# Optimization experiments

Hardware: AMD Instinct MI355X
Metric: run time of the kernel (lower is better)

## Reference

```python
import jax, jax.numpy as jnp
import numpy as np

RADIUS = 1.3
N_SAMPLES = 256
STEP = 0.0176


def trilinear(grid, pts):
    """grid: [C, D, H, W]; pts: [M, 3] in [-1, 1] ordered (x, y, z) like torch grid_sample
    (x indexes W, y indexes H, z indexes D), align_corners=True, border padding.
    Returns [M, C]."""
    C, D, H, W = grid.shape
    sizes = jnp.asarray([W, H, D], dtype=pts.dtype)
    co = jnp.clip((pts + 1.0) * 0.5 * (sizes - 1.0), 0.0, sizes - 1.0)
    c0 = jnp.floor(co)
    f = co - c0                                   # [M,3] trilinear weights
    i0 = c0.astype(jnp.int32)
    i1 = jnp.minimum(i0 + 1, jnp.asarray([W - 1, H - 1, D - 1], jnp.int32))
    gf = grid.reshape(C, -1)

    def gat(ix, iy, iz):                          # -> [M, C]
        return gf[:, (iz * H + iy) * W + ix].T

    x0, y0, z0 = i0[:, 0], i0[:, 1], i0[:, 2]
    x1, y1, z1 = i1[:, 0], i1[:, 1], i1[:, 2]
    wx, wy, wz = f[:, 0:1], f[:, 1:2], f[:, 2:3]
    out = (gat(x0, y0, z0) * (1 - wx) * (1 - wy) * (1 - wz)
         + gat(x1, y0, z0) * wx       * (1 - wy) * (1 - wz)
         + gat(x0, y1, z0) * (1 - wx) * wy       * (1 - wz)
         + gat(x1, y1, z0) * wx       * wy       * (1 - wz)
         + gat(x0, y0, z1) * (1 - wx) * (1 - wy) * wz
         + gat(x1, y0, z1) * wx       * (1 - wy) * wz
         + gat(x0, y1, z1) * (1 - wx) * wy       * wz
         + gat(x1, y1, z1) * wx       * wy       * wz)
    return out


def get_intersections(rays_o, dirn):
    """Ray / cube[-R,R]^3 intersection; N_SAMPLES uniform steps from entry point.
    Returns pts [B,N,3], t-values [B,N], validity mask [B,N]."""
    eps = 1e-9
    safe_d = jnp.where(jnp.abs(dirn) < eps, eps, dirn)
    inv = 1.0 / safe_d
    t1 = (-RADIUS - rays_o) * inv
    t2 = (RADIUS - rays_o) * inv
    tmin = jnp.max(jnp.minimum(t1, t2), axis=-1)
    tmax = jnp.min(jnp.maximum(t1, t2), axis=-1)
    tnear = jnp.maximum(tmin, 0.0)
    hit = tmax > tnear                                          # [B]
    t = tnear[:, None] + STEP * jnp.arange(N_SAMPLES, dtype=rays_o.dtype)[None, :]
    pts = rays_o[:, None, :] + t[..., None] * dirn[:, None, :]  # [B,N,3]
    mask = (t < tmax[:, None]) & hit[:, None]
    return pts, t, mask


def setup_inputs() -> dict:
    key = jax.random.key(0)
    ks = jax.random.split(key, 12)
    B, R, GD, FD, NF, HW = 2048, 128, 3, 32, 32, 64
    o = jax.random.normal(ks[0], (B, 3), dtype=jnp.float32)
    rays_o = o / jnp.linalg.norm(o, axis=-1, keepdims=True) * (2.0 * RADIUS)
    rays_d = -rays_o + 0.3 * jax.random.normal(ks[1], (B, 3), dtype=jnp.float32)
    G1 = 0.01 * jax.random.normal(ks[2], (GD, R, R, R), dtype=jnp.float32)
    F = 0.05 * jax.random.normal(ks[3], (FD, NF, NF, NF), dtype=jnp.float32)
    s = 0.1
    return {
        'rays_o': rays_o, 'rays_d': rays_d, 'G1': G1, 'F': F,
        'Wd1': s * jax.random.normal(ks[4], (FD, HW), dtype=jnp.float32),
        'bd1': jnp.zeros((HW,), jnp.float32),
        'Wd2': s * jax.random.normal(ks[5], (HW, 1), dtype=jnp.float32),
        'bd2': jnp.zeros((1,), jnp.float32),
        'Wc1': s * jax.random.normal(ks[6], (FD + 3, HW), dtype=jnp.float32),
        'bc1': jnp.zeros((HW,), jnp.float32),
        'Wc2': s * jax.random.normal(ks[7], (HW, 3), dtype=jnp.float32),
        'bc2': jnp.zeros((3,), jnp.float32),
    }


def reference(rays_o, rays_d, G1, F, Wd1, bd1, Wd2, bd2, Wc1, bc1, Wc2, bc2):
    B = rays_o.shape[0]
    dirn = rays_d / jnp.linalg.norm(rays_d, axis=-1, keepdims=True)
    pts, t, mask = get_intersections(rays_o, dirn)           # [B,N,3],[B,N],[B,N]
    pts_n = (pts / RADIUS).reshape(-1, 3)                     # [M,3] in ~[-1,1]

    # nested multi-grid trilinear lookups: coords -> G1 -> F
    g1v = trilinear(G1, pts_n)                                # [M,3]
    feats = trilinear(F, g1v)                                 # [M,feature_dim]

    # density MLP (1 hidden layer, width 64)
    h = jax.nn.relu(feats @ Wd1 + bd1)
    sigma = (h @ Wd2 + bd2)[:, 0].reshape(B, N_SAMPLES)
    sigma = jnp.where(mask, sigma, 0.0)

    # sigma -> alpha -> compositing weights (abs_light)
    dists = jnp.concatenate([t[:, 1:] - t[:, :-1],
                             jnp.full((B, 1), STEP, t.dtype)], axis=1)
    alpha = 1.0 - jnp.exp(-jax.nn.relu(sigma) * dists)
    T = jnp.cumprod(1.0 - alpha + 1e-10, axis=1)
    T_excl = jnp.concatenate([jnp.ones((B, 1), alpha.dtype), T[:, :-1]], axis=1)
    weights = alpha * T_excl                                  # [B,N]

    # color MLP conditioned on view direction
    dflat = jnp.broadcast_to(dirn[:, None, :], (B, N_SAMPLES, 3)).reshape(-1, 3)
    hc = jax.nn.relu(jnp.concatenate([feats, dflat], axis=-1) @ Wc1 + bc1)
    rgb = jax.nn.sigmoid((hc @ Wc2 + bc2).reshape(B, N_SAMPLES, 3))
    rgb = jnp.where(mask[..., None], rgb, 0.0)

    out = jnp.sum(weights[..., None] * rgb, axis=1)           # [B,3]
    acc = jnp.sum(weights, axis=1)
    return out + (1.0 - acc)[:, None]                         # white background
```

## Files before the change

### kernel.cpp

```cpp
#include <hip/hip_runtime.h>
#include <hip/hip_fp16.h>
#include <math.h>

#define NSAMP 256

typedef _Float16 f16;
typedef _Float16 f16x4 __attribute__((ext_vector_type(4)));
typedef _Float16 f16x8 __attribute__((ext_vector_type(8)));
typedef float    f32x4 __attribute__((ext_vector_type(4)));

__global__ __launch_bounds__(256) void transpose_F16(
    const float* __restrict__ Fg, f16* __restrict__ Ft)
{
    const int j = blockIdx.x * 256 + threadIdx.x;
    f16x8 o[4];
    #pragma unroll
    for (int q = 0; q < 4; ++q)
        #pragma unroll
        for (int i = 0; i < 8; ++i)
            o[q][i] = (f16)Fg[(size_t)(8*q+i)*32768 + j];
    f16* dst = Ft + (size_t)j * 32;
    #pragma unroll
    for (int q = 0; q < 4; ++q) *(f16x8*)(dst + q*8) = o[q];
    if (j == 32767) {
        f16x8 z = {};
        f16* pd = Ft + (size_t)32768 * 32;
        #pragma unroll
        for (int q = 0; q < 4; ++q) *(f16x8*)(pd + q*8) = z;
    }
}

__global__ __launch_bounds__(256) void transpose_G1p(
    const float* __restrict__ G1, f16x8* __restrict__ G1p)
{
    const int v  = blockIdx.x * 256 + threadIdx.x;
    const int vn = min(v + 1, 2097151);
    f16x8 o;
    o[0] = (f16)G1[v];
    o[1] = (f16)G1[2097152 + v];
    o[2] = (f16)G1[2*2097152 + v];
    o[3] = (f16)0.0f;
    o[4] = (f16)G1[vn];
    o[5] = (f16)G1[2097152 + vn];
    o[6] = (f16)G1[2*2097152 + vn];
    o[7] = (f16)0.0f;
    G1p[v] = o;
}

__global__ __launch_bounds__(256) void pack_bfrags(
    const float* __restrict__ Wd1, const float* __restrict__ Wc1,
    f16* __restrict__ Bd, f16* __restrict__ Bc)
{
    const int idx  = threadIdx.x;
    const int nt   = idx >> 6;
    const int lane = idx & 63;
    const int j    = nt*16 + (lane & 15);
    const int k0   = (lane >> 4) * 8;
    f16x8 vd, vc;
    #pragma unroll
    for (int i = 0; i < 8; ++i) {
        vd[i] = (f16)Wd1[(k0+i)*64 + j];
        vc[i] = (f16)Wc1[(k0+i)*64 + j];
    }
    *(f16x8*)(Bd + ((size_t)(nt*64+lane))*8) = vd;
    *(f16x8*)(Bc + ((size_t)(nt*64+lane))*8) = vc;
}

__global__ __launch_bounds__(256) __attribute__((amdgpu_waves_per_eu(2, 6)))
void nerf_fused_opt(
    const float* __restrict__ rays_o, const float* __restrict__ rays_d,
    const f16x8* __restrict__ G1p, const f16* __restrict__ Ft16,
    const float* __restrict__ bd1, const float* __restrict__ Wd2,
    const float* __restrict__ bd2,
    const float* __restrict__ Wc1, const float* __restrict__ bc1,
    const float* __restrict__ Wc2, const float* __restrict__ bc2,
    const f16* __restrict__ Bd, const f16* __restrict__ Bc,
    float* __restrict__ out)
{
    const float RADIUS = 1.3f;
    const float STEP = 0.0176f;

    const int b    = blockIdx.x;
    const int tid  = threadIdx.x;
    const int lane = tid & 63;
    const int wv   = tid >> 6;

    __shared__ __align__(16) f16 feats_lds[256][40];
    __shared__ float sig_lds[256];
    __shared__ f16   rgb_lds[256][4];
    __shared__ float s_wtot[4];
    __shared__ float s_red[4][4];

    const float ox = rays_o[b*3+0], oy = rays_o[b*3+1], oz = rays_o[b*3+2];
    const float rdx = rays_d[b*3+0], rdy = rays_d[b*3+1], rdz = rays_d[b*3+2];
    const float rn  = sqrtf(rdx*rdx + rdy*rdy + rdz*rdz);
    const float dxn = rdx/rn, dyn = rdy/rn, dzn = rdz/rn;

    float sd, inv, t1, t2, tmin, tmax;
    sd = (fabsf(dxn) < 1e-9f) ? 1e-9f : dxn; inv = 1.0f/sd;
    t1 = (-RADIUS - ox)*inv; t2 = (RADIUS - ox)*inv;
    tmin = fminf(t1,t2); tmax = fmaxf(t1,t2);
    sd = (fabsf(dyn) < 1e-9f) ? 1e-9f : dyn; inv = 1.0f/sd;
    t1 = (-RADIUS - oy)*inv; t2 = (RADIUS - oy)*inv;
    tmin = fmaxf(tmin, fminf(t1,t2)); tmax = fminf(tmax, fmaxf(t1,t2));
    sd = (fabsf(dzn) < 1e-9f) ? 1e-9f : dzn; inv = 1.0f/sd;
    t1 = (-RADIUS - oz)*inv; t2 = (RADIUS - oz)*inv;
    tmin = fmaxf(tmin, fminf(t1,t2)); tmax = fminf(tmax, fmaxf(t1,t2));

    const float tnear = fmaxf(tmin, 0.0f);
    const bool  hit   = tmax > tnear;
    const float t     = tnear + STEP * (float)tid;
    const bool  mask  = (t < tmax) && hit;

    const bool wave_active = __any(mask);

    float sigma = 0.0f, rr = 0.0f, rg = 0.0f, rb = 0.0f;

    float feats[32];
    if (wave_active) {
        const float invR = 1.0f / RADIUS;
        const float px = (ox + t*dxn) * invR;
        const float py = (oy + t*dyn) * invR;
        const float pz = (oz + t*dzn) * invR;

        float cox = fminf(fmaxf((px+1.0f)*0.5f*127.0f, 0.0f), 127.0f);
        float coy = fminf(fmaxf((py+1.0f)*0.5f*127.0f, 0.0f), 127.0f);
        float coz = fminf(fmaxf((pz+1.0f)*0.5f*127.0f, 0.0f), 127.0f);
        int x0 = (int)floorf(cox); float fx = cox - (float)x0;
        int y0 = (int)floorf(coy); float fy = coy - (float)y0; int y1 = min(y0+1, 127);
        int z0 = (int)floorf(coz); float fz = coz - (float)z0; int z1 = min(z0+1, 127);

        {
            const float wx0 = 1.0f-fx, wx1 = fx;
            const float wy0 = 1.0f-fy, wy1 = fy;
            const float wz0 = 1.0f-fz, wz1 = fz;
            const int i000 = (z0*128 + y0)*128 + x0;
            const int dyo = (y1 - y0)*128;
            const int dzo = (z1 - z0)*16384;

            const f16x8 p00 = G1p[i000];
            const f16x8 p10 = G1p[i000 + dyo];
            const f16x8 p01 = G1p[i000 + dzo];
            const f16x8 p11 = G1p[i000 + dyo + dzo];

            const float a00 = wy0*wz0, a10 = wy1*wz0, a01 = wy0*wz1, a11 = wy1*wz1;

            float g[3];
            #pragma unroll
            for (int c = 0; c < 3; ++c) {
                g[c] = a00*(wx0*(float)p00[c] + wx1*(float)p00[4+c])
                     + a10*(wx0*(float)p10[c] + wx1*(float)p10[4+c])
                     + a01*(wx0*(float)p01[c] + wx1*(float)p01[4+c])
                     + a11*(wx0*(float)p11[c] + wx1*(float)p11[4+c]);
            }

            cox = fminf(fmaxf((g[0]+1.0f)*0.5f*31.0f, 0.0f), 31.0f);
            coy = fminf(fmaxf((g[1]+1.0f)*0.5f*31.0f, 0.0f), 31.0f);
            coz = fminf(fmaxf((g[2]+1.0f)*0.5f*31.0f, 0.0f), 31.0f);
            x0 = (int)floorf(cox); fx = cox - (float)x0;
            y0 = (int)floorf(coy); fy = coy - (float)y0; y1 = min(y0+1, 31);
            z0 = (int)floorf(coz); fz = coz - (float)z0; z1 = min(z0+1, 31);
        }

        #pragma unroll
        for (int c = 0; c < 32; ++c) feats[c] = 0.0f;
        {
            const float wx0 = 1.0f-fx, wx1 = fx;
            const float wy0 = 1.0f-fy, wy1 = fy;
            const float wz0 = 1.0f-fz, wz1 = fz;
            const int j000 = (z0*32 + y0)*32 + x0;
            const int dyo = (y1 - y0)*32;
            const int dzo = (z1 - z0)*1024;

            const int   jp[4] = { j000, j000+dyo, j000+dzo, j000+dyo+dzo };
            const float ap[4] = { wy0*wz0, wy1*wz0, wy0*wz1, wy1*wz1 };

            #pragma unroll
            for (int p = 0; p < 4; ++p) {
                const f16* base = Ft16 + (size_t)jp[p] * 32;
                const float aw = ap[p]*wx0, bw = ap[p]*wx1;
                f16x8 lo[4], hi[4];
                #pragma unroll
                for (int q = 0; q < 4; ++q) lo[q] = *(const f16x8*)(base + q*8);
                #pragma unroll
                for (int q = 0; q < 4; ++q) hi[q] = *(const f16x8*)(base + 32 + q*8);
                #pragma unroll
                for (int q = 0; q < 4; ++q)
                    #pragma unroll
                    for (int i = 0; i < 8; ++i)
                        feats[8*q+i] += aw*(float)lo[q][i] + bw*(float)hi[q][i];
            }
        }
    }

    if (wave_active) {
        #pragma unroll
        for (int gq = 0; gq < 4; ++gq) {
            f16x8 h;
            #pragma unroll
            for (int i = 0; i < 8; ++i) h[i] = (f16)feats[gq*8+i];
            *(f16x8*)&feats_lds[tid][gq*8] = h;
        }
    }
    __syncthreads();

    if (wave_active) {
        const int lane15 = lane & 15;
        const int laneg  = lane >> 4;

        float bias_d[4], bias_c[4], wd2v[4];
        float wc2r[4], wc2g[4], wc2b[4];
        #pragma unroll
        for (int nt = 0; nt < 4; ++nt) {
            const int j = nt*16 + lane15;
            bias_d[nt] = bd1[j];
            bias_c[nt] = bc1[j] + dxn*Wc1[32*64+j] + dyn*Wc1[33*64+j] + dzn*Wc1[34*64+j];
            wd2v[nt]   = Wd2[j];
            wc2r[nt]   = Wc2[j*3+0];
            wc2g[nt]   = Wc2[j*3+1];
            wc2b[nt]   = Wc2[j*3+2];
        }
        f16x8 bdf[4], bcf[4];
        #pragma unroll
        for (int nt = 0; nt < 4; ++nt) {
            bdf[nt] = *(const f16x8*)(Bd + ((size_t)(nt*64+lane))*8);
            bcf[nt] = *(const f16x8*)(Bc + ((size_t)(nt*64+lane))*8);
        }

        #pragma unroll
        for (int mt = 0; mt < 4; ++mt) {
            const int arow = wv*64 + mt*16 + lane15;
            const f16x8 af = *(const f16x8*)&feats_lds[arow][laneg*8];

            f32x4 accd[4], accc[4];
            #pragma unroll
            for (int nt = 0; nt < 4; ++nt) {
                const float bdv = bias_d[nt], bcv = bias_c[nt];
                accd[nt] = (f32x4){bdv, bdv, bdv, bdv};
                accc[nt] = (f32x4){bcv, bcv, bcv, bcv};
            }
            #pragma unroll
            for (int nt = 0; nt < 4; ++nt) {
                accd[nt] = __builtin_amdgcn_mfma_f32_16x16x32_f16(af, bdf[nt], accd[nt], 0, 0, 0);
                accc[nt] = __builtin_amdgcn_mfma_f32_16x16x32_f16(af, bcf[nt], accc[nt], 0, 0, 0);
            }

            float ss[4] = {0.f,0.f,0.f,0.f};
            float sr[4] = {0.f,0.f,0.f,0.f};
            float sg[4] = {0.f,0.f,0.f,0.f};
            float sb[4] = {0.f,0.f,0.f,0.f};
            #pragma unroll
            for (int nt = 0; nt < 4; ++nt) {
                #pragma unroll
                for (int reg = 0; reg < 4; ++reg) {
                    const float hd = fmaxf(accd[nt][reg], 0.0f);
                    ss[reg] += hd * wd2v[nt];
                    const float hc = fmaxf(accc[nt][reg], 0.0f);
                    sr[reg] += hc * wc2r[nt];
                    sg[reg] += hc * wc2g[nt];
                    sb[reg] += hc * wc2b[nt];
                }
            }
            #pragma unroll
            for (int st = 1; st < 16; st <<= 1) {
                #pragma unroll
                for (int reg = 0; reg < 4; ++reg) {
                    ss[reg] += __shfl_xor(ss[reg], st, 64);
                    sr[reg] += __shfl_xor(sr[reg], st, 64);
                    sg[reg] += __shfl_xor(sg[reg], st, 64);
                    sb[reg] += __shfl_xor(sb[reg], st, 64);
                }
            }
            if (lane15 == 0) {
                const int base = wv*64 + mt*16 + laneg*4;
                #pragma unroll
                for (int reg = 0; reg < 4; ++reg) {
                    sig_lds[base+reg]    = ss[reg];
                    rgb_lds[base+reg][0] = (f16)sr[reg];
                    rgb_lds[base+reg][1] = (f16)sg[reg];
                    rgb_lds[base+reg][2] = (f16)sb[reg];
                }
            }
        }
    }
    __syncthreads();

    {
        const float sv  = sig_lds[tid];
        const float crv = (float)rgb_lds[tid][0] + bc2[0];
        const float cgv = (float)rgb_lds[tid][1] + bc2[1];
        const float cbv = (float)rgb_lds[tid][2] + bc2[2];
        sigma = mask ? (sv + bd2[0]) : 0.0f;
        rr = mask ? 1.0f/(1.0f + expf(-crv)) : 0.0f;
        rg = mask ? 1.0f/(1.0f + expf(-cgv)) : 0.0f;
        rb = mask ? 1.0f/(1.0f + expf(-cbv)) : 0.0f;
    }

    const float alpha = 1.0f - expf(-fmaxf(sigma, 0.0f) * STEP);
    float p = 1.0f - alpha + 1e-10f;

    float scan = p;
    #pragma unroll
    for (int off = 1; off < 64; off <<= 1) {
        const float n = __shfl_up(scan, off, 64);
        if (lane >= off) scan *= n;
    }
    if (lane == 63) s_wtot[wv] = scan;
    __syncthreads();

    float pre = 1.0f;
    #pragma unroll
    for (int q = 0; q < 4; ++q) if (q < wv) pre *= s_wtot[q];
    float excl = __shfl_up(scan, 1, 64);
    if (lane == 0) excl = 1.0f;
    const float Texcl = pre * excl;

    const float w = alpha * Texcl;
    float sw  = w;
    float swr = w * rr, swg = w * rg, swb = w * rb;

    #pragma unroll
    for (int off = 32; off > 0; off >>= 1) {
        sw  += __shfl_down(sw,  off, 64);
        swr += __shfl_down(swr, off, 64);
        swg += __shfl_down(swg, off, 64);
        swb += __shfl_down(swb, off, 64);
    }
    if (lane == 0) {
        s_red[wv][0] = sw;  s_red[wv][1] = swr;
        s_red[wv][2] = swg; s_red[wv][3] = swb;
    }
    __syncthreads();
    if (tid == 0) {
        float W = 0.0f, R = 0.0f, Gc = 0.0f, Bc_ = 0.0f;
        #pragma unroll
        for (int q = 0; q < 4; ++q) {
            W  += s_red[q][0]; R  += s_red[q][1];
            Gc += s_red[q][2]; Bc_ += s_red[q][3];
        }
        const float bg = 1.0f - W;
        out[b*3+0] = R   + bg;
        out[b*3+1] = Gc  + bg;
        out[b*3+2] = Bc_ + bg;
    }
}

__global__ __launch_bounds__(256) __attribute__((amdgpu_waves_per_eu(2, 6)))
void nerf_fused_naive(
    const float* __restrict__ rays_o, const float* __restrict__ rays_d,
    const float* __restrict__ G1, const float* __restrict__ Fg,
    const float* __restrict__ Wd1, const float* __restrict__ bd1,
    const float* __restrict__ Wd2, const float* __restrict__ bd2,
    const float* __restrict__ Wc1, const float* __restrict__ bc1,
    const float* __restrict__ Wc2, const float* __restrict__ bc2,
    float* __restrict__ out)
{
    const float RADIUS = 1.3f;
    const float STEP = 0.0176f;

    const int b    = blockIdx.x;
    const int tid  = threadIdx.x;
    const int lane = tid & 63;
    const int wv   = tid >> 6;

    __shared__ float s_wtot[4];
    __shared__ float s_red[4][4];

    const float ox = rays_o[b*3+0], oy = rays_o[b*3+1], oz = rays_o[b*3+2];
    const float rdx = rays_d[b*3+0], rdy = rays_d[b*3+1], rdz = rays_d[b*3+2];
    const float rn  = sqrtf(rdx*rdx + rdy*rdy + rdz*rdz);
    const float dxn = rdx/rn, dyn = rdy/rn, dzn = rdz/rn;

    float sd, inv, t1, t2, tmin, tmax;
    sd = (fabsf(dxn) < 1e-9f) ? 1e-9f : dxn; inv = 1.0f/sd;
    t1 = (-RADIUS - ox)*inv; t2 = (RADIUS - ox)*inv;
    tmin = fminf(t1,t2); tmax = fmaxf(t1,t2);
    sd = (fabsf(dyn) < 1e-9f) ? 1e-9f : dyn; inv = 1.0f/sd;
    t1 = (-RADIUS - oy)*inv; t2 = (RADIUS - oy)*inv;
    tmin = fmaxf(tmin, fminf(t1,t2)); tmax = fminf(tmax, fmaxf(t1,t2));
    sd = (fabsf(dzn) < 1e-9f) ? 1e-9f : dzn; inv = 1.0f/sd;
    t1 = (-RADIUS - oz)*inv; t2 = (RADIUS - oz)*inv;
    tmin = fmaxf(tmin, fminf(t1,t2)); tmax = fminf(tmax, fmaxf(t1,t2));

    const float tnear = fmaxf(tmin, 0.0f);
    const bool  hit   = tmax > tnear;
    const float t     = tnear + STEP * (float)tid;
    const bool  mask  = (t < tmax) && hit;

    float sigma = 0.0f, rr = 0.0f, rg = 0.0f, rb = 0.0f;

    if (__any(mask)) {
        const float invR = 1.0f / RADIUS;
        const float px = (ox + t*dxn) * invR;
        const float py = (oy + t*dyn) * invR;
        const float pz = (oz + t*dzn) * invR;

        float cox = fminf(fmaxf((px+1.0f)*0.5f*127.0f, 0.0f), 127.0f);
        float coy = fminf(fmaxf((py+1.0f)*0.5f*127.0f, 0.0f), 127.0f);
        float coz = fminf(fmaxf((pz+1.0f)*0.5f*127.0f, 0.0f), 127.0f);
        int x0 = (int)floorf(cox); float fx = cox - (float)x0; int x1 = min(x0+1, 127);
        int y0 = (int)floorf(coy); float fy = coy - (float)y0; int y1 = min(y0+1, 127);
        int z0 = (int)floorf(coz); float fz = coz - (float)z0; int z1 = min(z0+1, 127);

        float feats[32];
        {
            const float wx0 = 1.0f-fx, wx1 = fx;
            const float wy0 = 1.0f-fy, wy1 = fy;
            const float wz0 = 1.0f-fz, wz1 = fz;
            const float w000 = wx0*wy0*wz0, w100 = wx1*wy0*wz0;
            const float w010 = wx0*wy1*wz0, w110 = wx1*wy1*wz0;
            const float w001 = wx0*wy0*wz1, w101 = wx1*wy0*wz1;
            const float w011 = wx0*wy1*wz1, w111 = wx1*wy1*wz1;
            const int i000 = (z0*128 + y0)*128 + x0;
            const int dxo = x1 - x0;
            const int dyo = (y1 - y0)*128;
            const int dzo = (z1 - z0)*16384;
            const int i100 = i000 + dxo,       i010 = i000 + dyo;
            const int i110 = i000 + dyo + dxo, i001 = i000 + dzo;
            const int i101 = i000 + dzo + dxo, i011 = i000 + dzo + dyo;
            const int i111 = i000 + dzo + dyo + dxo;

            float g[3];
            #pragma unroll
            for (int c = 0; c < 3; ++c) {
                const float* gp = G1 + (size_t)c * 2097152;
                g[c] = w000*gp[i000] + w100*gp[i100] + w010*gp[i010] + w110*gp[i110]
                     + w001*gp[i001] + w101*gp[i101] + w011*gp[i011] + w111*gp[i111];
            }

            cox = fminf(fmaxf((g[0]+1.0f)*0.5f*31.0f, 0.0f), 31.0f);
            coy = fminf(fmaxf((g[1]+1.0f)*0.5f*31.0f, 0.0f), 31.0f);
            coz = fminf(fmaxf((g[2]+1.0f)*0.5f*31.0f, 0.0f), 31.0f);
            x0 = (int)floorf(cox); fx = cox - (float)x0; x1 = min(x0+1, 31);
            y0 = (int)floorf(coy); fy = coy - (float)y0; y1 = min(y0+1, 31);
            z0 = (int)floorf(coz); fz = coz - (float)z0; z1 = min(z0+1, 31);

            const float vx0 = 1.0f-fx, vx1 = fx;
            const float vy0 = 1.0f-fy, vy1 = fy;
            const float vz0 = 1.0f-fz, vz1 = fz;
            const float u000 = vx0*vy0*vz0, u100 = vx1*vy0*vz0;
            const float u010 = vx0*vy1*vz0, u110 = vx1*vy1*vz0;
            const float u001 = vx0*vy0*vz1, u101 = vx1*vy0*vz1;
            const float u011 = vx0*vy1*vz1, u111 = vx1*vy1*vz1;
            const int j000 = (z0*32 + y0)*32 + x0;
            const int exo = x1 - x0;
            const int eyo = (y1 - y0)*32;
            const int ezo = (z1 - z0)*1024;
            const int j100 = j000 + exo,       j010 = j000 + eyo;
            const int j110 = j000 + eyo + exo, j001 = j000 + ezo;
            const int j101 = j000 + ezo + exo, j011 = j000 + ezo + eyo;
            const int j111 = j000 + ezo + eyo + exo;

            #pragma unroll
            for (int c = 0; c < 32; ++c) {
                const float* fp = Fg + (size_t)c * 32768;
                feats[c] = u000*fp[j000] + u100*fp[j100] + u010*fp[j010] + u110*fp[j110]
                         + u001*fp[j001] + u101*fp[j101] + u011*fp[j011] + u111*fp[j111];
            }
        }

        float sg1 = bd2[0], cr = 0.0f, cg = 0.0f, cb = 0.0f;
        for (int j0 = 0; j0 < 64; j0 += 8) {
            float ad[8], ac[8];
            #pragma unroll
            for (int jj = 0; jj < 8; ++jj) {
                ad[jj] = bd1[j0+jj];
                ac[jj] = bc1[j0+jj] + dxn*Wc1[32*64 + j0 + jj]
                                    + dyn*Wc1[33*64 + j0 + jj]
                                    + dzn*Wc1[34*64 + j0 + jj];
            }
            #pragma unroll
            for (int k = 0; k < 32; ++k) {
                const float fv = feats[k];
                #pragma unroll
                for (int jj = 0; jj < 8; ++jj) {
                    ad[jj] += fv * Wd1[k*64 + j0 + jj];
                    ac[jj] += fv * Wc1[k*64 + j0 + jj];
                }
            }
            #pragma unroll
            for (int jj = 0; jj < 8; ++jj) {
                sg1 += fmaxf(ad[jj], 0.0f) * Wd2[j0+jj];
                const float hc = fmaxf(ac[jj], 0.0f);
                cr += hc * Wc2[(j0+jj)*3 + 0];
                cg += hc * Wc2[(j0+jj)*3 + 1];
                cb += hc * Wc2[(j0+jj)*3 + 2];
            }
        }
        cr += bc2[0]; cg += bc2[1]; cb += bc2[2];
        sigma = mask ? sg1 : 0.0f;
        rr = mask ? 1.0f/(1.0f + expf(-cr)) : 0.0f;
        rg = mask ? 1.0f/(1.0f + expf(-cg)) : 0.0f;
        rb = mask ? 1.0f/(1.0f + expf(-cb)) : 0.0f;
    }

    const float alpha = 1.0f - expf(-fmaxf(sigma, 0.0f) * STEP);
    float p = 1.0f - alpha + 1e-10f;

    float scan = p;
    #pragma unroll
    for (int off = 1; off < 64; off <<= 1) {
        const float n = __shfl_up(scan, off, 64);
        if (lane >= off) scan *= n;
    }
    if (lane == 63) s_wtot[wv] = scan;
    __syncthreads();

    float pre = 1.0f;
    #pragma unroll
    for (int q = 0; q < 4; ++q) if (q < wv) pre *= s_wtot[q];
    float excl = __shfl_up(scan, 1, 64);
    if (lane == 0) excl = 1.0f;
    const float Texcl = pre * excl;

    const float w = alpha * Texcl;
    float sw  = w;
    float swr = w * rr, swg = w * rg, swb = w * rb;

    #pragma unroll
    for (int off = 32; off > 0; off >>= 1) {
        sw  += __shfl_down(sw,  off, 64);
        swr += __shfl_down(swr, off, 64);
        swg += __shfl_down(swg, off, 64);
        swb += __shfl_down(swb, off, 64);
    }
    if (lane == 0) {
        s_red[wv][0] = sw;  s_red[wv][1] = swr;
        s_red[wv][2] = swg; s_red[wv][3] = swb;
    }
    __syncthreads();
    if (tid == 0) {
        float W = 0.0f, R = 0.0f, Gc = 0.0f, Bc_ = 0.0f;
        #pragma unroll
        for (int q = 0; q < 4; ++q) {
            W  += s_red[q][0]; R  += s_red[q][1];
            Gc += s_red[q][2]; Bc_ += s_red[q][3];
        }
        const float bg = 1.0f - W;
        out[b*3+0] = R   + bg;
        out[b*3+1] = Gc  + bg;
        out[b*3+2] = Bc_ + bg;
    }
}

extern "C" void kernel_launch(void* const* d_in, const int* in_sizes, int n_in,
                              void* d_out, int out_size, void* d_ws, size_t ws_size,
                              hipStream_t stream) {
    const float* rays_o = (const float*)d_in[0];
    const float* rays_d = (const float*)d_in[1];
    const float* G1     = (const float*)d_in[2];
    const float* Fg     = (const float*)d_in[3];
    const float* Wd1    = (const float*)d_in[4];
    const float* bd1    = (const float*)d_in[5];
    const float* Wd2    = (const float*)d_in[6];
    const float* bd2    = (const float*)d_in[7];
    const float* Wc1    = (const float*)d_in[8];
    const float* bc1    = (const float*)d_in[9];
    const float* Wc2    = (const float*)d_in[10];
    const float* bc2    = (const float*)d_in[11];
    float* out = (float*)d_out;

    const int B = in_sizes[0] / 3;
    const size_t ft16_bytes = (size_t)32769 * 32 * sizeof(f16);
    const size_t g1p_bytes  = (size_t)2097152 * sizeof(f16x8);
    const size_t bf_bytes   = (size_t)4 * 64 * 8 * sizeof(f16);

    if (ws_size >= ft16_bytes + g1p_bytes + 2*bf_bytes) {
        f16*   Ft16 = (f16*)d_ws;
        f16x8* G1p  = (f16x8*)((char*)d_ws + ft16_bytes);
        f16*   Bd   = (f16*)((char*)d_ws + ft16_bytes + g1p_bytes);
        f16*   Bc   = (f16*)((char*)d_ws + ft16_bytes + g1p_bytes + bf_bytes);
        transpose_F16<<<dim3(128), dim3(256), 0, stream>>>(Fg, Ft16);
        transpose_G1p<<<dim3(8192), dim3(256), 0, stream>>>(G1, G1p);
        pack_bfrags<<<dim3(1), dim3(256), 0, stream>>>(Wd1, Wc1, Bd, Bc);
        nerf_fused_opt<<<dim3(B), dim3(NSAMP), 0, stream>>>(
            rays_o, rays_d, G1p, Ft16, bd1, Wd2, bd2, Wc1, bc1, Wc2, bc2,
            Bd, Bc, out);
    } else {
        nerf_fused_naive<<<dim3(B), dim3(NSAMP), 0, stream>>>(
            rays_o, rays_d, G1, Fg, Wd1, bd1, Wd2, bd2, Wc1, bc1, Wc2, bc2, out);
    }
}
```

Before: 142.0 us.

## Halve G1 staging, accumulate features in packed fp16, drop barriers, fast exp

Stores the first grid as f16x4 per voxel instead of neighbour-paired f16x8. This halves the staging buffer and the transpose writes, at the cost of eight gathers instead of four. Feature interpolation accumulates in packed fp16 vectors, and the partial-sum reductions shuffle f16x2 pairs. The two block barriers around the LDS staging are removed, and expf becomes __expf. The fp16 accumulation loses precision, and removing the barriers depends on each wave touching only its own LDS rows.

```diff
diff --git a/kernel.cpp b/kernel.cpp
--- a/kernel.cpp
+++ b/kernel.cpp
@@ -5,6 +5,7 @@
 #define NSAMP 256
 
 typedef _Float16 f16;
+typedef _Float16 f16x2 __attribute__((ext_vector_type(2)));
 typedef _Float16 f16x4 __attribute__((ext_vector_type(4)));
 typedef _Float16 f16x8 __attribute__((ext_vector_type(8)));
 typedef float    f32x4 __attribute__((ext_vector_type(4)));
@@ -30,21 +31,16 @@
     }
 }
 
-__global__ __launch_bounds__(256) void transpose_G1p(
-    const float* __restrict__ G1, f16x8* __restrict__ G1p)
+__global__ __launch_bounds__(256) void transpose_G1h(
+    const float* __restrict__ G1, f16x4* __restrict__ G1h)
 {
-    const int v  = blockIdx.x * 256 + threadIdx.x;
-    const int vn = min(v + 1, 2097151);
-    f16x8 o;
+    const int v = blockIdx.x * 256 + threadIdx.x;
+    f16x4 o;
     o[0] = (f16)G1[v];
     o[1] = (f16)G1[2097152 + v];
     o[2] = (f16)G1[2*2097152 + v];
     o[3] = (f16)0.0f;
-    o[4] = (f16)G1[vn];
-    o[5] = (f16)G1[2097152 + vn];
-    o[6] = (f16)G1[2*2097152 + vn];
-    o[7] = (f16)0.0f;
-    G1p[v] = o;
+    G1h[v] = o;
 }
 
 __global__ __launch_bounds__(256) void pack_bfrags(
@@ -66,10 +62,17 @@
     *(f16x8*)(Bc + ((size_t)(nt*64+lane))*8) = vc;
 }
 
+__device__ inline f16x2 shfl_xor_h2(f16x2 v, int m) {
+    union { f16x2 h; int i; } u;
+    u.h = v;
+    u.i = __shfl_xor(u.i, m, 64);
+    return u.h;
+}
+
 __global__ __launch_bounds__(256) __attribute__((amdgpu_waves_per_eu(2, 6)))
 void nerf_fused_opt(
     const float* __restrict__ rays_o, const float* __restrict__ rays_d,
-    const f16x8* __restrict__ G1p, const f16* __restrict__ Ft16,
+    const f16x4* __restrict__ G1h, const f16* __restrict__ Ft16,
     const float* __restrict__ bd1, const float* __restrict__ Wd2,
     const float* __restrict__ bd2,
     const float* __restrict__ Wc1, const float* __restrict__ bc1,
@@ -116,7 +119,7 @@
 
     float sigma = 0.0f, rr = 0.0f, rg = 0.0f, rb = 0.0f;
 
-    float feats[32];
+    f16x8 facc[4];
     if (wave_active) {
         const float invR = 1.0f / RADIUS;
         const float px = (ox + t*dxn) * invR;
@@ -126,7 +129,7 @@
         float cox = fminf(fmaxf((px+1.0f)*0.5f*127.0f, 0.0f), 127.0f);
         float coy = fminf(fmaxf((py+1.0f)*0.5f*127.0f, 0.0f), 127.0f);
         float coz = fminf(fmaxf((pz+1.0f)*0.5f*127.0f, 0.0f), 127.0f);
-        int x0 = (int)floorf(cox); float fx = cox - (float)x0;
+        int x0 = (int)floorf(cox); float fx = cox - (float)x0; int x1 = min(x0+1, 127);
         int y0 = (int)floorf(coy); float fy = coy - (float)y0; int y1 = min(y0+1, 127);
         int z0 = (int)floorf(coz); float fz = coz - (float)z0; int z1 = min(z0+1, 127);
 
@@ -135,23 +138,31 @@
             const float wy0 = 1.0f-fy, wy1 = fy;
             const float wz0 = 1.0f-fz, wz1 = fz;
             const int i000 = (z0*128 + y0)*128 + x0;
+            const int dxo = x1 - x0;
             const int dyo = (y1 - y0)*128;
             const int dzo = (z1 - z0)*16384;
 
-            const f16x8 p00 = G1p[i000];
-            const f16x8 p10 = G1p[i000 + dyo];
-            const f16x8 p01 = G1p[i000 + dzo];
-            const f16x8 p11 = G1p[i000 + dyo + dzo];
-
-            const float a00 = wy0*wz0, a10 = wy1*wz0, a01 = wy0*wz1, a11 = wy1*wz1;
+            const f16x4 v000 = G1h[i000];
+            const f16x4 v100 = G1h[i000 + dxo];
+            const f16x4 v010 = G1h[i000 + dyo];
+            const f16x4 v110 = G1h[i000 + dyo + dxo];
+            const f16x4 v001 = G1h[i000 + dzo];
+            const f16x4 v101 = G1h[i000 + dzo + dxo];
+            const f16x4 v011 = G1h[i000 + dzo + dyo];
+            const f16x4 v111 = G1h[i000 + dzo + dyo + dxo];
+
+            const float w000 = wx0*wy0*wz0, w100 = wx1*wy0*wz0;
+            const float w010 = wx0*wy1*wz0, w110 = wx1*wy1*wz0;
+            const float w001 = wx0*wy0*wz1, w101 = wx1*wy0*wz1;
+            const float w011 = wx0*wy1*wz1, w111 = wx1*wy1*wz1;
 
             float g[3];
             #pragma unroll
             for (int c = 0; c < 3; ++c) {
-                g[c] = a00*(wx0*(float)p00[c] + wx1*(float)p00[4+c])
-                     + a10*(wx0*(float)p10[c] + wx1*(float)p10[4+c])
-                     + a01*(wx0*(float)p01[c] + wx1*(float)p01[4+c])
-                     + a11*(wx0*(float)p11[c] + wx1*(float)p11[4+c]);
+                g[c] = w000*(float)v000[c] + w100*(float)v100[c]
+                     + w010*(float)v010[c] + w110*(float)v110[c]
+                     + w001*(float)v001[c] + w101*(float)v101[c]
+                     + w011*(float)v011[c] + w111*(float)v111[c];
             }
 
             cox = fminf(fmaxf((g[0]+1.0f)*0.5f*31.0f, 0.0f), 31.0f);
@@ -162,8 +173,6 @@
             z0 = (int)floorf(coz); fz = coz - (float)z0; z1 = min(z0+1, 31);
         }
 
-        #pragma unroll
-        for (int c = 0; c < 32; ++c) feats[c] = 0.0f;
         {
             const float wx0 = 1.0f-fx, wx1 = fx;
             const float wy0 = 1.0f-fy, wy1 = fy;
@@ -176,33 +185,28 @@
             const float ap[4] = { wy0*wz0, wy1*wz0, wy0*wz1, wy1*wz1 };
 
             #pragma unroll
+            for (int q = 0; q < 4; ++q) facc[q] = (f16x8){};
+
+            #pragma unroll
             for (int p = 0; p < 4; ++p) {
                 const f16* base = Ft16 + (size_t)jp[p] * 32;
-                const float aw = ap[p]*wx0, bw = ap[p]*wx1;
-                f16x8 lo[4], hi[4];
+                const f16 ah = (f16)(ap[p]*wx0), bh = (f16)(ap[p]*wx1);
+                const f16x8 av = {ah,ah,ah,ah,ah,ah,ah,ah};
+                const f16x8 bv = {bh,bh,bh,bh,bh,bh,bh,bh};
                 #pragma unroll
-                for (int q = 0; q < 4; ++q) lo[q] = *(const f16x8*)(base + q*8);
-                #pragma unroll
-                for (int q = 0; q < 4; ++q) hi[q] = *(const f16x8*)(base + 32 + q*8);
-                #pragma unroll
-                for (int q = 0; q < 4; ++q)
-                    #pragma unroll
-                    for (int i = 0; i < 8; ++i)
-                        feats[8*q+i] += aw*(float)lo[q][i] + bw*(float)hi[q][i];
-            }
-        }
-    }
-
-    if (wave_active) {
-        #pragma unroll
-        for (int gq = 0; gq < 4; ++gq) {
-            f16x8 h;
-            #pragma unroll
-            for (int i = 0; i < 8; ++i) h[i] = (f16)feats[gq*8+i];
-            *(f16x8*)&feats_lds[tid][gq*8] = h;
-        }
-    }
-    __syncthreads();
+                for (int q = 0; q < 4; ++q) {
+                    const f16x8 lo = *(const f16x8*)(base + q*8);
+                    const f16x8 hi = *(const f16x8*)(base + 32 + q*8);
+                    facc[q] += av * lo;
+                    facc[q] += bv * hi;
+                }
+            }
+        }
+
+        #pragma unroll
+        for (int gq = 0; gq < 4; ++gq)
+            *(f16x8*)&feats_lds[tid][gq*8] = facc[gq];
+    }
 
     if (wave_active) {
         const int lane15 = lane & 15;
@@ -261,29 +265,32 @@
                     sb[reg] += hc * wc2b[nt];
                 }
             }
+            f16x2 pa[4], pb[4];
+            #pragma unroll
+            for (int reg = 0; reg < 4; ++reg) {
+                pa[reg] = (f16x2){(f16)ss[reg], (f16)sr[reg]};
+                pb[reg] = (f16x2){(f16)sg[reg], (f16)sb[reg]};
+            }
             #pragma unroll
             for (int st = 1; st < 16; st <<= 1) {
                 #pragma unroll
                 for (int reg = 0; reg < 4; ++reg) {
-                    ss[reg] += __shfl_xor(ss[reg], st, 64);
-                    sr[reg] += __shfl_xor(sr[reg], st, 64);
-                    sg[reg] += __shfl_xor(sg[reg], st, 64);
-                    sb[reg] += __shfl_xor(sb[reg], st, 64);
+                    pa[reg] += shfl_xor_h2(pa[reg], st);
+                    pb[reg] += shfl_xor_h2(pb[reg], st);
                 }
             }
             if (lane15 == 0) {
                 const int base = wv*64 + mt*16 + laneg*4;
                 #pragma unroll
                 for (int reg = 0; reg < 4; ++reg) {
-                    sig_lds[base+reg]    = ss[reg];
-                    rgb_lds[base+reg][0] = (f16)sr[reg];
-                    rgb_lds[base+reg][1] = (f16)sg[reg];
-                    rgb_lds[base+reg][2] = (f16)sb[reg];
+                    sig_lds[base+reg]    = (float)pa[reg][0];
+                    rgb_lds[base+reg][0] = pa[reg][1];
+                    rgb_lds[base+reg][1] = pb[reg][0];
+                    rgb_lds[base+reg][2] = pb[reg][1];
                 }
             }
         }
     }
-    __syncthreads();
 
     {
         const float sv  = sig_lds[tid];
@@ -291,12 +298,12 @@
         const float cgv = (float)rgb_lds[tid][1] + bc2[1];
         const float cbv = (float)rgb_lds[tid][2] + bc2[2];
         sigma = mask ? (sv + bd2[0]) : 0.0f;
-        rr = mask ? 1.0f/(1.0f + expf(-crv)) : 0.0f;
-        rg = mask ? 1.0f/(1.0f + expf(-cgv)) : 0.0f;
-        rb = mask ? 1.0f/(1.0f + expf(-cbv)) : 0.0f;
-    }
-
-    const float alpha = 1.0f - expf(-fmaxf(sigma, 0.0f) * STEP);
+        rr = mask ? 1.0f/(1.0f + __expf(-crv)) : 0.0f;
+        rg = mask ? 1.0f/(1.0f + __expf(-cgv)) : 0.0f;
+        rb = mask ? 1.0f/(1.0f + __expf(-cbv)) : 0.0f;
+    }
+
+    const float alpha = 1.0f - __expf(-fmaxf(sigma, 0.0f) * STEP);
     float p = 1.0f - alpha + 1e-10f;
 
     float scan = p;
@@ -562,19 +569,19 @@
 
     const int B = in_sizes[0] / 3;
     const size_t ft16_bytes = (size_t)32769 * 32 * sizeof(f16);
-    const size_t g1p_bytes  = (size_t)2097152 * sizeof(f16x8);
+    const size_t g1h_bytes  = (size_t)2097152 * sizeof(f16x4);
     const size_t bf_bytes   = (size_t)4 * 64 * 8 * sizeof(f16);
 
-    if (ws_size >= ft16_bytes + g1p_bytes + 2*bf_bytes) {
+    if (ws_size >= ft16_bytes + g1h_bytes + 2*bf_bytes) {
         f16*   Ft16 = (f16*)d_ws;
-        f16x8* G1p  = (f16x8*)((char*)d_ws + ft16_bytes);
-        f16*   Bd   = (f16*)((char*)d_ws + ft16_bytes + g1p_bytes);
-        f16*   Bc   = (f16*)((char*)d_ws + ft16_bytes + g1p_bytes + bf_bytes);
+        f16x4* G1h  = (f16x4*)((char*)d_ws + ft16_bytes);
+        f16*   Bd   = (f16*)((char*)d_ws + ft16_bytes + g1h_bytes);
+        f16*   Bc   = (f16*)((char*)d_ws + ft16_bytes + g1h_bytes + bf_bytes);
         transpose_F16<<<dim3(128), dim3(256), 0, stream>>>(Fg, Ft16);
-        transpose_G1p<<<dim3(8192), dim3(256), 0, stream>>>(G1, G1p);
+        transpose_G1h<<<dim3(8192), dim3(256), 0, stream>>>(G1, G1h);
         pack_bfrags<<<dim3(1), dim3(256), 0, stream>>>(Wd1, Wc1, Bd, Bc);
         nerf_fused_opt<<<dim3(B), dim3(NSAMP), 0, stream>>>(
-            rays_o, rays_d, G1p, Ft16, bd1, Wd2, bd2, Wc1, bc1, Wc2, bc2,
+            rays_o, rays_d, G1h, Ft16, bd1, Wd2, bd2, Wc1, bc1, Wc2, bc2,
             Bd, Bc, out);
     } else {
         nerf_fused_naive<<<dim3(B), dim3(NSAMP), 0, stream>>>(
```

After: 133.0 us. 1.07x faster.
